# Optimization experiments

Measured on AMD Instinct MI355X. Metric: run time of the kernel, lower is better.

Reference implementation:

```python
import jax, jax.numpy as jnp
import numpy as np

B, M, K, N = 4, 2048, 4096, 4096


def setup_inputs() -> dict:
    key = jax.random.key(0)
    k1, k2, k3, k4, k5 = jax.random.split(key, 5)
    # quantized activations in [-8, 7], stored as int8 (spec dtype int32, cast here)
    x_q = jax.random.randint(k1, (B, M, K), -8, 8, dtype=jnp.int32).astype(jnp.int8)
    # per-token activation scales (B, M, 1)
    scales_x = jax.random.uniform(k2, (B, M, 1), dtype=jnp.float32, minval=0.001, maxval=0.02)
    # int8 weight (N, K) in [-8, 7] as produced by from_float
    weight = jax.random.randint(k3, (N, K), -8, 8, dtype=jnp.int32).astype(jnp.int8)
    # per-output-row weight scales (N, 1)
    weight_scales = jax.random.uniform(k4, (N, 1), dtype=jnp.float32, minval=0.001, maxval=0.02)
    bias = jax.random.normal(k5, (N,), dtype=jnp.float32) * 0.02
    return {"x_q": x_q, "scales_x": scales_x, "weight": weight,
            "weight_scales": weight_scales, "bias": bias}


def reference(x_q, scales_x, weight, weight_scales, bias):
    acc = jnp.einsum('bmk,nk->bmn', x_q, weight,
                     preferred_element_type=jnp.int32)  # (B, M, N) int32
    # sym_dequant: per-token scale * per-row weight scale, then fused bias add
    out = acc.astype(jnp.float32) * scales_x * weight_scales.reshape(1, 1, N) + bias
    return out
```

## Files before the change

### kernel.cpp

```cpp
#include <hip/hip_runtime.h>
#include <stdint.h>

#define MROWS 8192
#define K_DIM 4096
#define N_DIM 4096
#define BM 256
#define BN 256
#define BK 64
#define KT (K_DIM / BK)
#define ABYTES (BM * BK)
#define TBYTES (2 * ABYTES)

#define X_ELEMS (MROWS * K_DIM)
#define W_ELEMS (N_DIM * K_DIM)

typedef __attribute__((ext_vector_type(4)))  int   int4v;
typedef __attribute__((ext_vector_type(16))) int   int16v;
typedef __attribute__((ext_vector_type(4)))  float float4v;

#define GLOAD_LDS16(gptr, lptr)                                                   \
    __builtin_amdgcn_global_load_lds((const __attribute__((address_space(1))) void*)(gptr), \
                                     (__attribute__((address_space(3))) void*)(lptr), 16, 0, 0)

__device__ __forceinline__ int pack4(int4v v) {
    return (int)((unsigned)(v[0] & 0xFF)
               | ((unsigned)(v[1] & 0xFF) << 8)
               | ((unsigned)(v[2] & 0xFF) << 16)
               | ((unsigned)(v[3] & 0xFF) << 24));
}

__global__ __launch_bounds__(256) void pack_i32_to_i8(
    const int4v* __restrict__ srcX, int* __restrict__ dstX, int n4x,
    const int4v* __restrict__ srcW, int* __restrict__ dstW, int n4w)
{
    const int stride = gridDim.x * blockDim.x;
    const int n4 = n4x + n4w;
    for (int i = blockIdx.x * blockDim.x + threadIdx.x; i < n4; i += stride) {
        if (i < n4x) dstX[i] = pack4(srcX[i]);
        else         dstW[i - n4x] = pack4(srcW[i - n4x]);
    }
}

__global__ __launch_bounds__(512, 2) void i8gemm_dq_kernel(
    const int8_t* __restrict__ xq,
    const float*  __restrict__ sx,
    const int8_t* __restrict__ wt,
    const float*  __restrict__ ws,
    const float*  __restrict__ bias,
    float*        __restrict__ out)
{
    __shared__ __align__(16) int8_t lds8[4 * TBYTES];

    const int tid  = threadIdx.x;
    const int wave = tid >> 6;
    const int lane = tid & 63;
    const int wr   = wave >> 2;
    const int wcn  = wave & 3;

    const int bid = blockIdx.x;
    const int wg  = (bid & 7) * 64 + (bid >> 3);
    const int ct  = wg & 15;
    const int rt  = wg >> 4;

    const int srow = wave * 16 + (lane >> 2);
    const int scol = (((lane & 3) - ((lane >> 3) & 3)) & 3) * 16;
    const int8_t* gA0 = xq + (size_t)(rt * BM + srow) * K_DIM + scol;
    const int8_t* gA1 = gA0 + (size_t)128 * K_DIM;
    const int8_t* gB0 = wt + (size_t)(ct * BN + srow) * K_DIM + scol;
    const int8_t* gB1 = gB0 + (size_t)128 * K_DIM;
    const int dA0 = wave * 1024;
    const int dA1 = 8192 + wave * 1024;
    const int dB0 = ABYTES + wave * 1024;
    const int dB1 = ABYTES + 8192 + wave * 1024;

    const int m32 = lane & 31;
    const int hi  = lane >> 5;
    const int askew = ((hi + (m32 >> 1)) & 3) * 16;
    const int aoff  = (wr * 128 + m32) * BK;
    const int boff  = ABYTES + (wcn * 64 + m32) * BK;

    int16v acc[4][2] = {};

    #pragma unroll
    for (int u = 0; u < 3; ++u) {
        const size_t ko = (size_t)u * BK;
        int8_t* bb = lds8 + u * TBYTES;
        GLOAD_LDS16(gA0 + ko, bb + dA0);
        GLOAD_LDS16(gA1 + ko, bb + dA1);
        GLOAD_LDS16(gB0 + ko, bb + dB0);
        GLOAD_LDS16(gB1 + ko, bb + dB1);
    }

    #pragma unroll 4
    for (int t = 0; t < KT; ++t) {
        const int  buf = t & 3;
        const int  nb  = (t + 3) & 3;
        const int  u   = (t + 3) & (KT - 1);
        const size_t ko = (size_t)u * BK;
        const int8_t* base = lds8 + buf * TBYTES;
        int8_t* nbb = lds8 + nb * TBYTES;

        asm volatile("s_waitcnt vmcnt(8)" ::: "memory");
        __builtin_amdgcn_s_barrier();
        __builtin_amdgcn_sched_barrier(0);

        int4v a0[2][2], bf[2][2];
        #pragma unroll
        for (int i = 0; i < 2; ++i)
            #pragma unroll
            for (int s = 0; s < 2; ++s)
                a0[i][s] = *(const int4v*)(base + aoff + i * 2048 + (askew ^ (s << 5)));
        #pragma unroll
        for (int j = 0; j < 2; ++j)
            #pragma unroll
            for (int s = 0; s < 2; ++s)
                bf[j][s] = *(const int4v*)(base + boff + j * 2048 + (askew ^ (s << 5)));
        GLOAD_LDS16(gA0 + ko, nbb + dA0);
        GLOAD_LDS16(gA1 + ko, nbb + dA1);

        __builtin_amdgcn_s_setprio(1);
        #pragma unroll
        for (int s = 0; s < 2; ++s)
            #pragma unroll
            for (int i = 0; i < 2; ++i)
                #pragma unroll
                for (int j = 0; j < 2; ++j)
                    acc[i][j] = __builtin_amdgcn_mfma_i32_32x32x32_i8(
                                    a0[i][s], bf[j][s], acc[i][j], 0, 0, 0);
        __builtin_amdgcn_s_setprio(0);

        int4v a1[2][2];
        #pragma unroll
        for (int i = 0; i < 2; ++i)
            #pragma unroll
            for (int s = 0; s < 2; ++s)
                a1[i][s] = *(const int4v*)(base + aoff + (2 + i) * 2048 + (askew ^ (s << 5)));
        GLOAD_LDS16(gB0 + ko, nbb + dB0);
        GLOAD_LDS16(gB1 + ko, nbb + dB1);

        __builtin_amdgcn_s_setprio(1);
        #pragma unroll
        for (int s = 0; s < 2; ++s)
            #pragma unroll
            for (int i = 0; i < 2; ++i)
                #pragma unroll
                for (int j = 0; j < 2; ++j)
                    acc[2 + i][j] = __builtin_amdgcn_mfma_i32_32x32x32_i8(
                                        a1[i][s], bf[j][s], acc[2 + i][j], 0, 0, 0);
        __builtin_amdgcn_s_setprio(0);
    }

    asm volatile("s_waitcnt vmcnt(0)" ::: "memory");

    const int row_base = rt * BM + wr * 128;
    const int col_base = ct * BN + wcn * 64;

    float wsc[2], bsc[2];
    #pragma unroll
    for (int j = 0; j < 2; ++j) {
        const int c = col_base + j * 32 + m32;
        wsc[j] = ws[c];
        bsc[j] = bias[c];
    }

    #pragma unroll
    for (int i = 0; i < 4; ++i) {
        #pragma unroll
        for (int q = 0; q < 4; ++q) {
            const int r0 = row_base + i * 32 + q * 8 + hi * 4;
            const float4v sx4 = *(const float4v*)(sx + r0);
            #pragma unroll
            for (int j = 0; j < 2; ++j) {
                const int c = col_base + j * 32 + m32;
                float* o = out + (size_t)r0 * N_DIM + c;
                #pragma unroll
                for (int r = 0; r < 4; ++r)
                    o[(size_t)r * N_DIM] = (float)acc[i][j][q * 4 + r] * sx4[r] * wsc[j] + bsc[j];
            }
        }
    }
}

extern "C" void kernel_launch(void* const* d_in, const int* in_sizes, int n_in,
                              void* d_out, int out_size, void* d_ws, size_t ws_size,
                              hipStream_t stream) {
    const int*   xq32 = (const int*)d_in[0];
    const float* sx   = (const float*)d_in[1];
    const int*   wt32 = (const int*)d_in[2];
    const float* ws   = (const float*)d_in[3];
    const float* bias = (const float*)d_in[4];
    float* out = (float*)d_out;

    int8_t* xq8 = (int8_t*)d_ws;
    int8_t* wt8 = xq8 + (size_t)X_ELEMS;

    {
        int n4x = X_ELEMS / 4;
        int n4w = W_ELEMS / 4;
        pack_i32_to_i8<<<2048, 256, 0, stream>>>((const int4v*)xq32, (int*)xq8, n4x,
                                                 (const int4v*)wt32, (int*)wt8, n4w);
    }

    dim3 grid((MROWS / BM) * (N_DIM / BN));
    i8gemm_dq_kernel<<<grid, 512, 0, stream>>>(xq8, sx, wt8, ws, bias, out);
}
```

Baseline: 404.0 us.

## Restructure LDS tile layout for conflict-free direct loads and widen int8 packing

Changes the global-to-LDS staging so each wave loads 32 rows in two 1KB half-K chunks, giving a contiguous per-row 16-byte layout that the MFMA operand reads hit with simple offsets instead of an XOR skew. The pack kernel now handles 16 elements per thread with 128-bit stores, launched as two separate full grids for activations and weights instead of one grid-stride loop. The layout change aims to make LDS reads and async loads cheaper. The new global access pattern touches 32 rows per wave, which may reduce coalescing, and the unskewed reads may cause bank conflicts.

```diff
diff --git a/kernel.cpp b/kernel.cpp
--- a/kernel.cpp
+++ b/kernel.cpp
@@ -30,15 +30,17 @@
 }
 
 __global__ __launch_bounds__(256) void pack_i32_to_i8(
-    const int4v* __restrict__ srcX, int* __restrict__ dstX, int n4x,
-    const int4v* __restrict__ srcW, int* __restrict__ dstW, int n4w)
+    const int4v* __restrict__ src, int4v* __restrict__ dst, int n16)
 {
-    const int stride = gridDim.x * blockDim.x;
-    const int n4 = n4x + n4w;
-    for (int i = blockIdx.x * blockDim.x + threadIdx.x; i < n4; i += stride) {
-        if (i < n4x) dstX[i] = pack4(srcX[i]);
-        else         dstW[i - n4x] = pack4(srcW[i - n4x]);
-    }
+    int i = blockIdx.x * blockDim.x + threadIdx.x;
+    if (i >= n16) return;
+    int4v a = src[4 * i + 0];
+    int4v b = src[4 * i + 1];
+    int4v c = src[4 * i + 2];
+    int4v d = src[4 * i + 3];
+    int4v r;
+    r[0] = pack4(a); r[1] = pack4(b); r[2] = pack4(c); r[3] = pack4(d);
+    dst[i] = r;
 }
 
 __global__ __launch_bounds__(512, 2) void i8gemm_dq_kernel(
@@ -62,33 +64,33 @@
     const int ct  = wg & 15;
     const int rt  = wg >> 4;
 
-    const int srow = wave * 16 + (lane >> 2);
-    const int scol = (((lane & 3) - ((lane >> 3) & 3)) & 3) * 16;
-    const int8_t* gA0 = xq + (size_t)(rt * BM + srow) * K_DIM + scol;
-    const int8_t* gA1 = gA0 + (size_t)128 * K_DIM;
-    const int8_t* gB0 = wt + (size_t)(ct * BN + srow) * K_DIM + scol;
-    const int8_t* gB1 = gB0 + (size_t)128 * K_DIM;
-    const int dA0 = wave * 1024;
-    const int dA1 = 8192 + wave * 1024;
-    const int dB0 = ABYTES + wave * 1024;
-    const int dB1 = ABYTES + 8192 + wave * 1024;
-
-    const int m32 = lane & 31;
-    const int hi  = lane >> 5;
-    const int askew = ((hi + (m32 >> 1)) & 3) * 16;
-    const int aoff  = (wr * 128 + m32) * BK;
-    const int boff  = ABYTES + (wcn * 64 + m32) * BK;
+    const int sr = lane & 31;
+    const int sc = (lane >> 5) * 16;
+    const int8_t* gA = xq + (size_t)(rt * BM + wave * 32 + sr) * K_DIM + sc;
+    const int8_t* gB = wt + (size_t)(ct * BN + wave * 32 + sr) * K_DIM + sc;
+    const int dA = wave * 2048;
+    const int dB = ABYTES + wave * 2048;
+
+    const int m32  = lane & 31;
+    const int hi   = lane >> 5;
+    const int rb   = hi * 512 + m32 * 16;
+    const int aoff = (wr * 4) * 2048 + rb;
+    const int boff = ABYTES + (wcn * 2) * 2048 + rb;
 
     int16v acc[4][2] = {};
+
+#define STAGE_A(U, BB) { const size_t ko_ = (size_t)(U) * BK;   \
+        GLOAD_LDS16(gA + ko_,      (BB) + dA);                  \
+        GLOAD_LDS16(gA + ko_ + 32, (BB) + dA + 1024); }
+#define STAGE_B(U, BB) { const size_t ko_ = (size_t)(U) * BK;   \
+        GLOAD_LDS16(gB + ko_,      (BB) + dB);                  \
+        GLOAD_LDS16(gB + ko_ + 32, (BB) + dB + 1024); }
 
     #pragma unroll
     for (int u = 0; u < 3; ++u) {
-        const size_t ko = (size_t)u * BK;
         int8_t* bb = lds8 + u * TBYTES;
-        GLOAD_LDS16(gA0 + ko, bb + dA0);
-        GLOAD_LDS16(gA1 + ko, bb + dA1);
-        GLOAD_LDS16(gB0 + ko, bb + dB0);
-        GLOAD_LDS16(gB1 + ko, bb + dB1);
+        STAGE_A(u, bb);
+        STAGE_B(u, bb);
     }
 
     #pragma unroll 4
@@ -96,7 +98,6 @@
         const int  buf = t & 3;
         const int  nb  = (t + 3) & 3;
         const int  u   = (t + 3) & (KT - 1);
-        const size_t ko = (size_t)u * BK;
         const int8_t* base = lds8 + buf * TBYTES;
         int8_t* nbb = lds8 + nb * TBYTES;
 
@@ -109,14 +110,13 @@
         for (int i = 0; i < 2; ++i)
             #pragma unroll
             for (int s = 0; s < 2; ++s)
-                a0[i][s] = *(const int4v*)(base + aoff + i * 2048 + (askew ^ (s << 5)));
+                a0[i][s] = *(const int4v*)(base + aoff + i * 2048 + s * 1024);
         #pragma unroll
         for (int j = 0; j < 2; ++j)
             #pragma unroll
             for (int s = 0; s < 2; ++s)
-                bf[j][s] = *(const int4v*)(base + boff + j * 2048 + (askew ^ (s << 5)));
-        GLOAD_LDS16(gA0 + ko, nbb + dA0);
-        GLOAD_LDS16(gA1 + ko, nbb + dA1);
+                bf[j][s] = *(const int4v*)(base + boff + j * 2048 + s * 1024);
+        STAGE_A(u, nbb);
 
         __builtin_amdgcn_s_setprio(1);
         #pragma unroll
@@ -134,9 +134,8 @@
         for (int i = 0; i < 2; ++i)
             #pragma unroll
             for (int s = 0; s < 2; ++s)
-                a1[i][s] = *(const int4v*)(base + aoff + (2 + i) * 2048 + (askew ^ (s << 5)));
-        GLOAD_LDS16(gB0 + ko, nbb + dB0);
-        GLOAD_LDS16(gB1 + ko, nbb + dB1);
+                a1[i][s] = *(const int4v*)(base + aoff + (2 + i) * 2048 + s * 1024);
+        STAGE_B(u, nbb);
 
         __builtin_amdgcn_s_setprio(1);
         #pragma unroll
@@ -149,6 +148,9 @@
                                         a1[i][s], bf[j][s], acc[2 + i][j], 0, 0, 0);
         __builtin_amdgcn_s_setprio(0);
     }
+
+#undef STAGE_A
+#undef STAGE_B
 
     asm volatile("s_waitcnt vmcnt(0)" ::: "memory");
 
@@ -195,10 +197,10 @@
     int8_t* wt8 = xq8 + (size_t)X_ELEMS;
 
     {
-        int n4x = X_ELEMS / 4;
-        int n4w = W_ELEMS / 4;
-        pack_i32_to_i8<<<2048, 256, 0, stream>>>((const int4v*)xq32, (int*)xq8, n4x,
-                                                 (const int4v*)wt32, (int*)wt8, n4w);
+        int n16x = X_ELEMS / 16;
+        int n16w = W_ELEMS / 16;
+        pack_i32_to_i8<<<n16x / 256, 256, 0, stream>>>((const int4v*)xq32, (int4v*)xq8, n16x);
+        pack_i32_to_i8<<<n16w / 256, 256, 0, stream>>>((const int4v*)wt32, (int4v*)wt8, n16w);
     }
 
     dim3 grid((MROWS / BM) * (N_DIM / BN));
```

Result: slower. 425.1 us (+5.2%).
